# Kernel optimization log

Measured on AMD Instinct MI355X. Metric: run time of the kernel, lower is better.

Reference implementation:

```python
import jax, jax.numpy as jnp
import numpy as np

# DeepSeek-V2-Lite MoE dims
E = 64      # n_routed_experts
H = 2048    # hidden_size
I = 1408    # moe_intermediate_size
K = 6       # num_experts_per_tok (top-k)
T = 1024    # tokens
C = 256     # per-expert capacity (expected load T*K/E = 96; 256 is ample, no drops with seed 0)


def setup_inputs() -> dict:
    key = jax.random.key(0)
    k1, k2, k3, k4 = jax.random.split(key, 4)
    return {
        "hidden_states": jax.random.normal(k1, (T, H), jnp.float32),
        "gate_w": jax.random.normal(k2, (H, E), jnp.float32) * 0.02,   # LiteLinear(H->E), no bias
        "w1": jax.random.normal(k3, (E, H, I), jnp.float32) * 0.02,    # experts_w1
        "w2": jax.random.normal(k4, (E, I, H), jnp.float32) * 0.02,    # experts_w2
    }


def _moe(x, gate_w, w1, w2):
    # Router: softmax gate + top-k + renormalize (vLLM fused_moe renormalize=True)
    logits = x @ gate_w                                    # [T, E]
    probs = jax.nn.softmax(logits, axis=-1)
    topk_w, topk_idx = jax.lax.top_k(probs, K)             # [T, K]
    topk_w = topk_w / jnp.sum(topk_w, axis=-1, keepdims=True)

    # Dispatch: flatten (token, k) pairs, compute slot position within each expert
    P = T * K
    e_p = topk_idx.reshape(P)                              # expert id per pair
    onehot = (e_p[:, None] == jnp.arange(E)[None, :]).astype(jnp.int32)  # [P, E]
    pos = jnp.cumsum(onehot, axis=0) - 1                   # running count per expert
    pos = jnp.take_along_axis(pos, e_p[:, None], axis=1)[:, 0]           # [P]
    valid = pos < C
    pos_c = jnp.where(valid, pos, 0)
    fvalid = valid[:, None].astype(x.dtype)

    x_pair = jnp.repeat(x, K, axis=0)                      # [P, H]
    xe = jnp.zeros((E, C, H), x.dtype).at[e_p, pos_c].add(x_pair * fvalid)  # [E, C, H]

    # Grouped expert GEMMs: silu(x @ w1) @ w2
    h = jax.nn.silu(jnp.einsum('ech,ehi->eci', xe, w1))    # [E, C, I]
    ye = jnp.einsum('eci,eih->ech', h, w2)                 # [E, C, H]

    # Combine: gather back per pair, weight by routing prob, sum over k
    y_pair = ye[e_p, pos_c] * fvalid                       # [P, H]
    out = (y_pair.reshape(T, K, H) * topk_w[..., None]).sum(axis=1)
    return out


def reference(hidden_states, gate_w, w1, w2):
    return _moe(hidden_states, gate_w, w1, w2)
```

## Files before the change

### kernel.cpp

```cpp
#include <hip/hip_runtime.h>

#define T_TOK 1024
#define H_DIM 2048
#define I_DIM 1408
#define E_NUM 64
#define K_TOP 6
#define CAP   256
#define P_NUM (T_TOK * K_TOP)
#define ROWS_MAX 7168

typedef __bf16 bf16x8 __attribute__((ext_vector_type(8)));
typedef float  f32x4  __attribute__((ext_vector_type(4)));
typedef unsigned int uint32x2 __attribute__((ext_vector_type(2)));

__device__ inline unsigned pack2bf16(float a, float b) {
    unsigned short au = __builtin_bit_cast(unsigned short, (__bf16)a);
    unsigned short bu = __builtin_bit_cast(unsigned short, (__bf16)b);
    return (unsigned)au | ((unsigned)bu << 16);
}

__global__ void zero_out_kernel(float* __restrict__ out) {
    int i = blockIdx.x * 256 + threadIdx.x;
    ((f32x4*)out)[i] = (f32x4){0.f, 0.f, 0.f, 0.f};
}

__global__ void zerocnt_kernel(int* __restrict__ cnt) {
    if (threadIdx.x < E_NUM) cnt[threadIdx.x] = 0;
}

__global__ __launch_bounds__(256) void router_kernel(
        const float* __restrict__ x, const float* __restrict__ gw,
        float* __restrict__ tw, int* __restrict__ ti, __bf16* __restrict__ xb)
{
    const int t0  = blockIdx.x * 4;
    const int tid = threadIdx.x;
    __shared__ float xs[4][H_DIM];
    __shared__ float part[4][4][E_NUM];

    #pragma unroll
    for (int tt = 0; tt < 4; ++tt) {
        #pragma unroll
        for (int i = 0; i < 8; ++i) {
            float v = x[(size_t)(t0 + tt) * H_DIM + i * 256 + tid];
            xs[tt][i * 256 + tid] = v;
            xb[(size_t)(t0 + tt) * H_DIM + i * 256 + tid] = (__bf16)v;
        }
    }
    __syncthreads();

    const int e = tid & 63, q = tid >> 6;
    float a0 = 0.f, a1 = 0.f, a2 = 0.f, a3 = 0.f;
    for (int hh = q * 512; hh < q * 512 + 512; ++hh) {
        float g = gw[hh * E_NUM + e];
        a0 += xs[0][hh] * g; a1 += xs[1][hh] * g;
        a2 += xs[2][hh] * g; a3 += xs[3][hh] * g;
    }
    part[q][0][e] = a0; part[q][1][e] = a1; part[q][2][e] = a2; part[q][3][e] = a3;
    __syncthreads();

    const int tt = q;
    float l = part[0][tt][e] + part[1][tt][e] + part[2][tt][e] + part[3][tt][e];
    float m = l;
    #pragma unroll
    for (int s = 32; s; s >>= 1) m = fmaxf(m, __shfl_xor(m, s));
    float p = __expf(l - m);
    float sum = p;
    #pragma unroll
    for (int s = 32; s; s >>= 1) sum += __shfl_xor(sum, s);
    float prob = p / sum;

    float v = prob, wsum = 0.f;
    float tv[K_TOP]; int tix[K_TOP];
    #pragma unroll
    for (int k = 0; k < K_TOP; ++k) {
        float bv = v; int bi = e;
        #pragma unroll
        for (int s = 32; s; s >>= 1) {
            float ov = __shfl_xor(bv, s); int oi = __shfl_xor(bi, s);
            if (ov > bv || (ov == bv && oi < bi)) { bv = ov; bi = oi; }
        }
        tv[k] = bv; tix[k] = bi; wsum += bv;
        if (e == bi) v = -1.0f;
    }
    if (e == 0) {
        #pragma unroll
        for (int k = 0; k < K_TOP; ++k) {
            tw[(t0 + tt) * K_TOP + k] = tv[k] / wsum;
            ti[(t0 + tt) * K_TOP + k] = tix[k];
        }
    }
}

__global__ void dispatch_kernel(const int* __restrict__ ti, int* __restrict__ cnt,
                                int* __restrict__ list) {
    int p = blockIdx.x * 256 + threadIdx.x;
    if (p < P_NUM) {
        int e = ti[p];
        int slot = atomicAdd(&cnt[e], 1);
        if (slot < CAP) list[e * CAP + slot] = p;
    }
}

__global__ void scan_kernel(const int* __restrict__ cnt, int* __restrict__ base) {
    if (threadIdx.x == 0) {
        int acc = 0;
        for (int e = 0; e < E_NUM; ++e) {
            base[e] = acc;
            int c = cnt[e]; if (c > CAP) c = CAP;
            acc += (c + 15) & ~15;
        }
    }
}

#define B_LDB 36

__global__ __launch_bounds__(256, 3) void gemm1_kernel(
        const float* __restrict__ w1, const __bf16* __restrict__ xb,
        const int* __restrict__ cnt, const int* __restrict__ base,
        const int* __restrict__ list, __bf16* __restrict__ hbuf)
{
    const int e  = blockIdx.z;
    const int m0 = blockIdx.y * 128;
    const int nb = blockIdx.x * 128;

    int rows = cnt[e]; if (rows > CAP) rows = CAP;
    const int rows_pad = (rows + 15) & ~15;
    if (m0 >= rows_pad) return;
    int mcount = rows_pad - m0; if (mcount > 128) mcount = 128;
    const int nmf = mcount >> 4;
    const int hb = base[e];

    __shared__ __attribute__((aligned(16))) __bf16 As[128][72];
    __shared__ __attribute__((aligned(16))) unsigned Bs[128 * B_LDB];
    __shared__ int ts[128];

    const int tid = threadIdx.x;
    if (tid < 128) {
        int slot = m0 + tid;
        ts[tid] = (slot < rows) ? (list[e * CAP + slot] / K_TOP) : 0;
    }
    __syncthreads();

    const int lane = tid & 63;
    const int wv   = tid >> 6;
    const int l15  = lane & 15;
    const int lg   = lane >> 4;

    const int sm = tid >> 3;
    const int sk = (tid & 7) << 3;
    const __bf16* ap[4];
    #pragma unroll
    for (int it = 0; it < 4; ++it)
        ap[it] = xb + (size_t)ts[it * 32 + sm] * H_DIM + sk;

    const int c4 = tid & 31;
    const int kb = tid >> 5;
    const int Xw = 4 * ((c4 ^ (c4 >> 3)) & 7);
    const float* bload = w1 + (size_t)e * H_DIM * I_DIM + (nb + 4 * c4);

    int cB0 = wv * 32 + l15;
    int cB1 = cB0 + 16;
    int c4r0 = cB0 >> 2, c4r1 = cB1 >> 2;
    const int Xr0 = 4 * ((c4r0 ^ (c4r0 >> 3)) & 7);
    const int Xr1 = 4 * ((c4r1 ^ (c4r1 >> 3)) & 7);
    const unsigned* bfp0 = Bs + cB0 * B_LDB;
    const unsigned* bfp1 = Bs + cB1 * B_LDB;

    f32x4 acc[8][2];
    #pragma unroll
    for (int m = 0; m < 8; ++m) {
        acc[m][0] = (f32x4){0.f, 0.f, 0.f, 0.f};
        acc[m][1] = (f32x4){0.f, 0.f, 0.f, 0.f};
    }

    for (int k0 = 0; k0 < H_DIM; k0 += 64) {
        f32x4 f[8];
        const float* bp = bload + (size_t)(k0 + 4 * kb) * I_DIM;
        #pragma unroll
        for (int r = 0; r < 4; ++r) f[r] = *(const f32x4*)(bp + (size_t)r * I_DIM);
        const float* bp2 = bp + (size_t)32 * I_DIM;
        #pragma unroll
        for (int r = 0; r < 4; ++r) f[4 + r] = *(const f32x4*)(bp2 + (size_t)r * I_DIM);
        bf16x8 av[4];
        #pragma unroll
        for (int it = 0; it < 4; ++it) av[it] = *(const bf16x8*)(ap[it] + k0);

        __syncthreads();
        #pragma unroll
        for (int it = 0; it < 4; ++it)
            *(bf16x8*)(&As[it * 32 + sm][sk]) = av[it];
        #pragma unroll
        for (int b = 0; b < 2; ++b) {
            #pragma unroll
            for (int i = 0; i < 4; ++i) {
                unsigned lo = pack2bf16(f[4 * b + 0][i], f[4 * b + 1][i]);
                unsigned hi = pack2bf16(f[4 * b + 2][i], f[4 * b + 3][i]);
                int c = 4 * c4 + i;
                int p = 2 * kb + 16 * b;
                *(uint32x2*)(&Bs[c * B_LDB + (p ^ Xw)]) = (uint32x2){lo, hi};
            }
        }
        __syncthreads();

        #pragma unroll
        for (int ks = 0; ks < 2; ++ks) {
            int pbase = ks * 16 + lg * 4;
            bf16x8 b0 = *(const bf16x8*)(bfp0 + (pbase ^ Xr0));
            bf16x8 b1 = *(const bf16x8*)(bfp1 + (pbase ^ Xr1));
            #pragma unroll
            for (int m = 0; m < 8; ++m) {
                if (m < nmf) {
                    bf16x8 a = *(const bf16x8*)(&As[m * 16 + l15][ks * 32 + lg * 8]);
                    acc[m][0] = __builtin_amdgcn_mfma_f32_16x16x32_bf16(a, b0, acc[m][0], 0, 0, 0);
                    acc[m][1] = __builtin_amdgcn_mfma_f32_16x16x32_bf16(a, b1, acc[m][1], 0, 0, 0);
                }
            }
        }
    }

    const int nw = nb + wv * 32;
    #pragma unroll
    for (int m = 0; m < 8; ++m) {
        if (m < nmf) {
            #pragma unroll
            for (int nf = 0; nf < 2; ++nf) {
                #pragma unroll
                for (int j = 0; j < 4; ++j) {
                    int row = m * 16 + lg * 4 + j;
                    int col = nw + nf * 16 + l15;
                    float v = acc[m][nf][j];
                    float s = v / (1.0f + __expf(-v));
                    hbuf[(size_t)(hb + m0 + row) * I_DIM + col] = (__bf16)s;
                }
            }
        }
    }
}

__global__ __launch_bounds__(256, 3) void gemm2_kernel(
        const float* __restrict__ w2, const __bf16* __restrict__ hbuf,
        const int* __restrict__ cnt, const int* __restrict__ base,
        const int* __restrict__ list, const float* __restrict__ tw,
        float* __restrict__ out)
{
    const int e  = blockIdx.z;
    const int m0 = blockIdx.y * 128;
    const int nb = blockIdx.x * 128;

    int rows = cnt[e]; if (rows > CAP) rows = CAP;
    const int rows_pad = (rows + 15) & ~15;
    if (m0 >= rows_pad) return;
    int mcount = rows_pad - m0; if (mcount > 128) mcount = 128;
    const int nmf = mcount >> 4;
    const int hb = base[e];

    __shared__ __attribute__((aligned(16))) __bf16 As[128][72];
    __shared__ __attribute__((aligned(16))) unsigned Bs[128 * B_LDB];
    __shared__ int ps[128];
    __shared__ float tws[128];

    const int tid = threadIdx.x;
    if (tid < 128) {
        int slot = m0 + tid;
        int p = (slot < rows) ? list[e * CAP + slot] : -1;
        ps[tid] = p;
        tws[tid] = (p >= 0) ? tw[p] : 0.f;
    }

    const int lane = tid & 63;
    const int wv   = tid >> 6;
    const int l15  = lane & 15;
    const int lg   = lane >> 4;

    const int sm = tid >> 3;
    const int sk = (tid & 7) << 3;
    const __bf16* abase = hbuf + (size_t)(hb + m0 + sm) * I_DIM + sk;

    const int c4 = tid & 31;
    const int kb = tid >> 5;
    const int Xw = 4 * ((c4 ^ (c4 >> 3)) & 7);
    const float* bload = w2 + (size_t)e * I_DIM * H_DIM + (nb + 4 * c4);

    int cB0 = wv * 32 + l15;
    int cB1 = cB0 + 16;
    int c4r0 = cB0 >> 2, c4r1 = cB1 >> 2;
    const int Xr0 = 4 * ((c4r0 ^ (c4r0 >> 3)) & 7);
    const int Xr1 = 4 * ((c4r1 ^ (c4r1 >> 3)) & 7);
    const unsigned* bfp0 = Bs + cB0 * B_LDB;
    const unsigned* bfp1 = Bs + cB1 * B_LDB;

    f32x4 acc[8][2];
    #pragma unroll
    for (int m = 0; m < 8; ++m) {
        acc[m][0] = (f32x4){0.f, 0.f, 0.f, 0.f};
        acc[m][1] = (f32x4){0.f, 0.f, 0.f, 0.f};
    }

    for (int k0 = 0; k0 < I_DIM; k0 += 64) {
        f32x4 f[8];
        const float* bp = bload + (size_t)(k0 + 4 * kb) * H_DIM;
        #pragma unroll
        for (int r = 0; r < 4; ++r) f[r] = *(const f32x4*)(bp + (size_t)r * H_DIM);
        const float* bp2 = bp + (size_t)32 * H_DIM;
        #pragma unroll
        for (int r = 0; r < 4; ++r) f[4 + r] = *(const f32x4*)(bp2 + (size_t)r * H_DIM);
        bf16x8 av[4];
        #pragma unroll
        for (int it = 0; it < 4; ++it)
            av[it] = *(const bf16x8*)(abase + (size_t)(it * 32) * I_DIM + k0);

        __syncthreads();
        #pragma unroll
        for (int it = 0; it < 4; ++it)
            *(bf16x8*)(&As[it * 32 + sm][sk]) = av[it];
        #pragma unroll
        for (int b = 0; b < 2; ++b) {
            #pragma unroll
            for (int i = 0; i < 4; ++i) {
                unsigned lo = pack2bf16(f[4 * b + 0][i], f[4 * b + 1][i]);
                unsigned hi = pack2bf16(f[4 * b + 2][i], f[4 * b + 3][i]);
                int c = 4 * c4 + i;
                int p = 2 * kb + 16 * b;
                *(uint32x2*)(&Bs[c * B_LDB + (p ^ Xw)]) = (uint32x2){lo, hi};
            }
        }
        __syncthreads();

        #pragma unroll
        for (int ks = 0; ks < 2; ++ks) {
            int pbase = ks * 16 + lg * 4;
            bf16x8 b0 = *(const bf16x8*)(bfp0 + (pbase ^ Xr0));
            bf16x8 b1 = *(const bf16x8*)(bfp1 + (pbase ^ Xr1));
            #pragma unroll
            for (int m = 0; m < 8; ++m) {
                if (m < nmf) {
                    bf16x8 a = *(const bf16x8*)(&As[m * 16 + l15][ks * 32 + lg * 8]);
                    acc[m][0] = __builtin_amdgcn_mfma_f32_16x16x32_bf16(a, b0, acc[m][0], 0, 0, 0);
                    acc[m][1] = __builtin_amdgcn_mfma_f32_16x16x32_bf16(a, b1, acc[m][1], 0, 0, 0);
                }
            }
        }
    }

    const int nw = nb + wv * 32;
    #pragma unroll
    for (int m = 0; m < 8; ++m) {
        if (m < nmf) {
            #pragma unroll
            for (int nf = 0; nf < 2; ++nf) {
                #pragma unroll
                for (int j = 0; j < 4; ++j) {
                    int row = m * 16 + lg * 4 + j;
                    int p = ps[row];
                    if (p >= 0) {
                        int t = p / K_TOP;
                        float v = acc[m][nf][j] * tws[row];
                        atomicAdd(&out[(size_t)t * H_DIM + (nw + nf * 16 + l15)], v);
                    }
                }
            }
        }
    }
}

extern "C" void kernel_launch(void* const* d_in, const int* in_sizes, int n_in,
                              void* d_out, int out_size, void* d_ws, size_t ws_size,
                              hipStream_t stream) {
    const float* x  = (const float*)d_in[0];
    const float* gw = (const float*)d_in[1];
    const float* w1 = (const float*)d_in[2];
    const float* w2 = (const float*)d_in[3];
    float* out = (float*)d_out;

    char* ws = (char*)d_ws;
    int*    cnt  = (int*)ws;
    int*    base = (int*)(ws + 256);
    int*    list = (int*)(ws + 512);
    float*  tw   = (float*)(ws + 66048);
    int*    ti   = (int*)(ws + 90624);
    __bf16* xb   = (__bf16*)(ws + 131072);
    __bf16* hbuf = (__bf16*)(ws + 4325376);

    hipLaunchKernelGGL(zero_out_kernel, dim3(T_TOK * H_DIM / 4 / 256), dim3(256), 0, stream, out);
    hipLaunchKernelGGL(zerocnt_kernel, dim3(1), dim3(64), 0, stream, cnt);
    hipLaunchKernelGGL(router_kernel, dim3(T_TOK / 4), dim3(256), 0, stream,
                       x, gw, tw, ti, xb);
    hipLaunchKernelGGL(dispatch_kernel, dim3((P_NUM + 255) / 256), dim3(256), 0, stream,
                       ti, cnt, list);
    hipLaunchKernelGGL(scan_kernel, dim3(1), dim3(64), 0, stream, cnt, base);
    hipLaunchKernelGGL(gemm1_kernel, dim3(I_DIM / 128, 2, E_NUM), dim3(256), 0, stream,
                       w1, xb, cnt, base, list, hbuf);
    hipLaunchKernelGGL(gemm2_kernel, dim3(H_DIM / 128, 2, E_NUM), dim3(256), 0, stream,
                       w2, hbuf, cnt, base, list, tw, out);
}
```

Measured before the change: 464.9 us.

## Prefetch next K-tile in expert GEMMs and fuse dispatch/scan into one kernel

Both grouped GEMM kernels now issue global loads for the next 64-wide K slice (fp32 weights and bf16 activations) into registers right after writing the current slice to LDS. This lets memory latency overlap with the MFMA work of the current slice. Separately, the zero-count, dispatch and scan kernels are merged into one single-block kernel that counts with LDS atomics, which removes two launches. The cost is higher register pressure under launch_bounds(256,3), and a serial single-block dispatch.

After: 448.8 us. 1.04x faster.

```diff
diff --git a/kernel.cpp b/kernel.cpp
--- a/kernel.cpp
+++ b/kernel.cpp
@@ -7,7 +7,6 @@
 #define K_TOP 6
 #define CAP   256
 #define P_NUM (T_TOK * K_TOP)
-#define ROWS_MAX 7168
 
 typedef __bf16 bf16x8 __attribute__((ext_vector_type(8)));
 typedef float  f32x4  __attribute__((ext_vector_type(4)));
@@ -22,10 +21,6 @@
 __global__ void zero_out_kernel(float* __restrict__ out) {
     int i = blockIdx.x * 256 + threadIdx.x;
     ((f32x4*)out)[i] = (f32x4){0.f, 0.f, 0.f, 0.f};
-}
-
-__global__ void zerocnt_kernel(int* __restrict__ cnt) {
-    if (threadIdx.x < E_NUM) cnt[threadIdx.x] = 0;
 }
 
 __global__ __launch_bounds__(256) void router_kernel(
@@ -91,22 +86,29 @@
     }
 }
 
-__global__ void dispatch_kernel(const int* __restrict__ ti, int* __restrict__ cnt,
-                                int* __restrict__ list) {
-    int p = blockIdx.x * 256 + threadIdx.x;
-    if (p < P_NUM) {
+__global__ __launch_bounds__(1024) void dispatch_scan_kernel(
+        const int* __restrict__ ti, int* __restrict__ cnt,
+        int* __restrict__ base, int* __restrict__ list)
+{
+    __shared__ int lcnt[E_NUM];
+    const int tid = threadIdx.x;
+    if (tid < E_NUM) lcnt[tid] = 0;
+    __syncthreads();
+    #pragma unroll
+    for (int i = 0; i < P_NUM / 1024; ++i) {
+        int p = i * 1024 + tid;
         int e = ti[p];
-        int slot = atomicAdd(&cnt[e], 1);
+        int slot = atomicAdd(&lcnt[e], 1);
         if (slot < CAP) list[e * CAP + slot] = p;
     }
-}
-
-__global__ void scan_kernel(const int* __restrict__ cnt, int* __restrict__ base) {
-    if (threadIdx.x == 0) {
+    __syncthreads();
+    if (tid == 0) {
         int acc = 0;
         for (int e = 0; e < E_NUM; ++e) {
             base[e] = acc;
-            int c = cnt[e]; if (c > CAP) c = CAP;
+            int c = lcnt[e];
+            cnt[e] = c;
+            if (c > CAP) c = CAP;
             acc += (c + 15) & ~15;
         }
     }
@@ -173,18 +175,20 @@
         acc[m][1] = (f32x4){0.f, 0.f, 0.f, 0.f};
     }
 
-    for (int k0 = 0; k0 < H_DIM; k0 += 64) {
-        f32x4 f[8];
-        const float* bp = bload + (size_t)(k0 + 4 * kb) * I_DIM;
+    f32x4 f[8]; bf16x8 av[4];
+    {
+        const float* bp = bload + (size_t)(4 * kb) * I_DIM;
         #pragma unroll
         for (int r = 0; r < 4; ++r) f[r] = *(const f32x4*)(bp + (size_t)r * I_DIM);
         const float* bp2 = bp + (size_t)32 * I_DIM;
         #pragma unroll
         for (int r = 0; r < 4; ++r) f[4 + r] = *(const f32x4*)(bp2 + (size_t)r * I_DIM);
-        bf16x8 av[4];
-        #pragma unroll
-        for (int it = 0; it < 4; ++it) av[it] = *(const bf16x8*)(ap[it] + k0);
-
+        #pragma unroll
+        for (int it = 0; it < 4; ++it) av[it] = *(const bf16x8*)(ap[it]);
+    }
+
+    for (int k0 = 0; k0 < H_DIM; k0 += 64) {
+        int kn = k0 + 64; if (kn >= H_DIM) kn = 0;
         __syncthreads();
         #pragma unroll
         for (int it = 0; it < 4; ++it)
@@ -200,8 +204,17 @@
                 *(uint32x2*)(&Bs[c * B_LDB + (p ^ Xw)]) = (uint32x2){lo, hi};
             }
         }
+        {
+            const float* bp = bload + (size_t)(kn + 4 * kb) * I_DIM;
+            #pragma unroll
+            for (int r = 0; r < 4; ++r) f[r] = *(const f32x4*)(bp + (size_t)r * I_DIM);
+            const float* bp2 = bp + (size_t)32 * I_DIM;
+            #pragma unroll
+            for (int r = 0; r < 4; ++r) f[4 + r] = *(const f32x4*)(bp2 + (size_t)r * I_DIM);
+            #pragma unroll
+            for (int it = 0; it < 4; ++it) av[it] = *(const bf16x8*)(ap[it] + kn);
+        }
         __syncthreads();
-
         #pragma unroll
         for (int ks = 0; ks < 2; ++ks) {
             int pbase = ks * 16 + lg * 4;
@@ -296,19 +309,21 @@
         acc[m][1] = (f32x4){0.f, 0.f, 0.f, 0.f};
     }
 
-    for (int k0 = 0; k0 < I_DIM; k0 += 64) {
-        f32x4 f[8];
-        const float* bp = bload + (size_t)(k0 + 4 * kb) * H_DIM;
+    f32x4 f[8]; bf16x8 av[4];
+    {
+        const float* bp = bload + (size_t)(4 * kb) * H_DIM;
         #pragma unroll
         for (int r = 0; r < 4; ++r) f[r] = *(const f32x4*)(bp + (size_t)r * H_DIM);
         const float* bp2 = bp + (size_t)32 * H_DIM;
         #pragma unroll
         for (int r = 0; r < 4; ++r) f[4 + r] = *(const f32x4*)(bp2 + (size_t)r * H_DIM);
-        bf16x8 av[4];
         #pragma unroll
         for (int it = 0; it < 4; ++it)
-            av[it] = *(const bf16x8*)(abase + (size_t)(it * 32) * I_DIM + k0);
-
+            av[it] = *(const bf16x8*)(abase + (size_t)(it * 32) * I_DIM);
+    }
+
+    for (int k0 = 0; k0 < I_DIM; k0 += 64) {
+        int kn = k0 + 64; if (kn >= I_DIM) kn = 0;
         __syncthreads();
         #pragma unroll
         for (int it = 0; it < 4; ++it)
@@ -323,6 +338,17 @@
                 int p = 2 * kb + 16 * b;
                 *(uint32x2*)(&Bs[c * B_LDB + (p ^ Xw)]) = (uint32x2){lo, hi};
             }
+        }
+        {
+            const float* bp = bload + (size_t)(kn + 4 * kb) * H_DIM;
+            #pragma unroll
+            for (int r = 0; r < 4; ++r) f[r] = *(const f32x4*)(bp + (size_t)r * H_DIM);
+            const float* bp2 = bp + (size_t)32 * H_DIM;
+            #pragma unroll
+            for (int r = 0; r < 4; ++r) f[4 + r] = *(const f32x4*)(bp2 + (size_t)r * H_DIM);
+            #pragma unroll
+            for (int it = 0; it < 4; ++it)
+                av[it] = *(const bf16x8*)(abase + (size_t)(it * 32) * I_DIM + kn);
         }
         __syncthreads();
 
@@ -382,12 +408,10 @@
     __bf16* hbuf = (__bf16*)(ws + 4325376);
 
     hipLaunchKernelGGL(zero_out_kernel, dim3(T_TOK * H_DIM / 4 / 256), dim3(256), 0, stream, out);
-    hipLaunchKernelGGL(zerocnt_kernel, dim3(1), dim3(64), 0, stream, cnt);
     hipLaunchKernelGGL(router_kernel, dim3(T_TOK / 4), dim3(256), 0, stream,
                        x, gw, tw, ti, xb);
-    hipLaunchKernelGGL(dispatch_kernel, dim3((P_NUM + 255) / 256), dim3(256), 0, stream,
-                       ti, cnt, list);
-    hipLaunchKernelGGL(scan_kernel, dim3(1), dim3(64), 0, stream, cnt, base);
+    hipLaunchKernelGGL(dispatch_scan_kernel, dim3(1), dim3(1024), 0, stream,
+                       ti, cnt, base, list);
     hipLaunchKernelGGL(gemm1_kernel, dim3(I_DIM / 128, 2, E_NUM), dim3(256), 0, stream,
                        w1, xb, cnt, base, list, hbuf);
     hipLaunchKernelGGL(gemm2_kernel, dim3(H_DIM / 128, 2, E_NUM), dim3(256), 0, stream,
```
